# Kernel tuning notes

Measured on AMD Instinct MI355X. Metric: run time of the kernel, lower is better.

## Reference

```python
import jax, jax.numpy as jnp
import numpy as np

B, H, W = 16, 128, 128
CIN, HID, OUT = 1, 64, 1
WS, NH = 8, 4  # window size, num heads
HD = HID // NH  # head dim = 16


def setup_inputs() -> dict:
    key = jax.random.key(0)
    ks = jax.random.split(key, 32)
    s = 0.05
    d = {"x": jax.random.normal(ks[0], (B, H, W, CIN), jnp.float32)}
    ins = [CIN, HID]
    for l in range(2):
        cin = ins[l]
        kb = 1 + 7 * l
        d[f"conv_w{l}"] = jax.random.normal(ks[kb], (4 * HID, cin + HID, 3, 3), jnp.float32) * s
        d[f"conv_b{l}"] = jnp.zeros((4 * HID,), jnp.float32)
        d[f"px_w{l}"] = jax.random.normal(ks[kb + 1], (HID, cin, 3, 3), jnp.float32) * s
        d[f"py_w{l}"] = jax.random.normal(ks[kb + 2], (HID, cin, 3, 3), jnp.float32) * s
        d[f"qkv_w{l}"] = jax.random.normal(ks[kb + 3], (3 * HID, HID), jnp.float32) * s
        d[f"proj_w{l}"] = jax.random.normal(ks[kb + 4], (HID, HID), jnp.float32) * s
        d[f"proj_b{l}"] = jnp.zeros((HID,), jnp.float32)
    d["out_w"] = jax.random.normal(ks[20], (OUT, HID, 1, 1), jnp.float32) * s
    d["out_b"] = jnp.zeros((OUT,), jnp.float32)
    return d


def _conv(x, w, pad, b=None):
    y = jax.lax.conv_general_dilated(
        x, w, (1, 1), [(pad, pad), (pad, pad)],
        dimension_numbers=("NCHW", "OIHW", "NCHW"))
    if b is not None:
        y = y + b[None, :, None, None]
    return y


def _win_attn(x, qkv_w, proj_w, proj_b):
    # x: [B, H, W, C], H and W are multiples of WS (pad branch is a no-op)
    Bx, Hx, Wx, C = x.shape
    nw_h, nw_w = Hx // WS, Wx // WS
    xw = x.reshape(Bx, nw_h, WS, nw_w, WS, C).transpose(0, 1, 3, 2, 4, 5)
    xw = xw.reshape(-1, WS * WS, C)  # [N, T, C], N = B*nw_h*nw_w, T = 64
    qkv = (xw @ qkv_w.T).reshape(-1, WS * WS, 3, NH, HD).transpose(2, 0, 3, 1, 4)
    q, k, v = qkv[0], qkv[1], qkv[2]  # [N, NH, T, HD]
    attn = jax.nn.softmax(jnp.einsum("nhqd,nhkd->nhqk", q, k) * (HD ** -0.5), axis=-1)
    o = jnp.einsum("nhqk,nhkd->nhqd", attn, v).transpose(0, 2, 1, 3).reshape(-1, WS * WS, C)
    o = o @ proj_w.T + proj_b
    o = o.reshape(Bx, nw_h, nw_w, WS, WS, C).transpose(0, 1, 3, 2, 4, 5)
    return o.reshape(Bx, Hx, Wx, C)


def _cell(x, h, c, cw, cb, pxw, pyw, qw, pw, pb):
    # x: [B, Cin, H, W]; h, c: [B, HID, H, W]
    cc = _conv(jnp.concatenate([x, h], axis=1), cw, 1, cb)
    ci, cf, co, cg = jnp.split(cc, 4, axis=1)
    px = _conv(x, pxw, 1)
    py = _conv(x, pyw, 1)
    i = jax.nn.sigmoid(ci + px)
    f = jax.nn.sigmoid(cf + px)
    o = jax.nn.sigmoid(co + py)
    g = jnp.tanh(cg + py)
    c2 = f * c + i * g
    h2 = o * jnp.tanh(c2)
    h2 = _win_attn(h2.transpose(0, 2, 3, 1), qw, pw, pb).transpose(0, 3, 1, 2)
    return h2, c2


def reference(x, conv_w0, conv_b0, px_w0, py_w0, qkv_w0, proj_w0, proj_b0,
              conv_w1, conv_b1, px_w1, py_w1, qkv_w1, proj_w1, proj_b1,
              out_w, out_b):
    # 4D input path: [B,H,W,C] -> NCHW frame, seq_len = 1
    xin = x.transpose(0, 3, 1, 2)
    z = jnp.zeros((B, HID, H, W), x.dtype)
    h0, _ = _cell(xin, z, z, conv_w0, conv_b0, px_w0, py_w0, qkv_w0, proj_w0, proj_b0)
    h1, _ = _cell(h0, z, z, conv_w1, conv_b1, px_w1, py_w1, qkv_w1, proj_w1, proj_b1)
    out = _conv(h1, out_w, 0, out_b)  # 1x1 output conv on last layer's (T=1) output
    return out.transpose(0, 2, 3, 1)  # [B, H, W, OUT]
```

## Files before the change

### kernel.cpp

```cpp
#include <hip/hip_runtime.h>


#define DEVFN __device__ __forceinline__

typedef __attribute__((ext_vector_type(8))) short short8;
typedef __attribute__((ext_vector_type(4))) float f32x4;

DEVFN float sigmoidf_(float z) { return 1.0f / (1.0f + __expf(-z)); }

DEVFN float tanhf_(float x) {
    float e = __expf(2.0f * x);
    return 1.0f - 2.0f / (e + 1.0f);
}

DEVFN unsigned short f2bf(float f) {
    unsigned int u = __builtin_bit_cast(unsigned int, f);
    u += 0x7fffu + ((u >> 16) & 1u);
    return (unsigned short)(u >> 16);
}

DEVFN unsigned pkbf(float a, float b) {
    return (unsigned)f2bf(a) | ((unsigned)f2bf(b) << 16);
}

__global__ __launch_bounds__(256) void repack_kernel(
    const float* __restrict__ cw0, const float* __restrict__ pxw0, const float* __restrict__ pyw0,
    const float* __restrict__ cw1, const float* __restrict__ pxw1, const float* __restrict__ pyw1,
    const float* __restrict__ qkvw0, const float* __restrict__ projw0,
    const float* __restrict__ qkvw1, const float* __restrict__ projw1,
    unsigned short* __restrict__ pwc, float* __restrict__ pw0,
    unsigned short* __restrict__ qb0, unsigned short* __restrict__ pjb0,
    unsigned short* __restrict__ qb1, unsigned short* __restrict__ pjb1)
{
    int idx = blockIdx.x * 256 + threadIdx.x;
    if (idx < 184320) {
        int j = idx & 7;
        int lane = (idx >> 3) & 63;
        int wv = (idx >> 9) & 3;
        int t = idx >> 11;
        int kk = t % 18, g = t / 18;
        int c = wv * 16 + (lane & 15);
        int kcol = kk * 32 + (lane >> 4) * 8 + j;
        int pos = kcol >> 6, cin = kcol & 63;
        float v;
        if (g == 0)      v = cw1[((c      ) * 128 + cin) * 9 + pos];
        else if (g == 1) v = cw1[((128 + c) * 128 + cin) * 9 + pos];
        else if (g == 2) v = cw1[((192 + c) * 128 + cin) * 9 + pos];
        else if (g == 3) v = pxw1[(c * 64 + cin) * 9 + pos];
        else             v = pyw1[(c * 64 + cin) * 9 + pos];
        pwc[idx] = f2bf(v);
    } else if (idx < 187200) {
        int i2 = idx - 184320;
        int g = i2 / (9 * 64);
        int rem = i2 - g * (9 * 64);
        int pos = rem >> 6, c = rem & 63;
        float v;
        if (g == 0)      v = cw0[(c      ) * 585 + pos];
        else if (g == 1) v = cw0[(128 + c) * 585 + pos];
        else if (g == 2) v = cw0[(192 + c) * 585 + pos];
        else if (g == 3) v = pxw0[c * 9 + pos];
        else             v = pyw0[c * 9 + pos];
        pw0[i2] = v;
    } else if (idx < 187200 + 12288) {
        int i = idx - 187200;           qb0[i] = f2bf(qkvw0[i]);
    } else if (idx < 187200 + 24576) {
        int i = idx - 187200 - 12288;   qb1[i] = f2bf(qkvw1[i]);
    } else if (idx < 187200 + 24576 + 4096) {
        int i = idx - 187200 - 24576;   pjb0[i] = f2bf(projw0[i]);
    } else if (idx < 187200 + 24576 + 8192) {
        int i = idx - 187200 - 28672;   pjb1[i] = f2bf(projw1[i]);
    }
}

__global__ __launch_bounds__(256) void gates1_kernel(
    const float* __restrict__ x, const float* __restrict__ pw,
    const float* __restrict__ cb, unsigned short* __restrict__ dst)
{
    const int idx = blockIdx.x * 256 + threadIdx.x;
    const int pix = idx >> 4, ch0 = (idx & 15) * 4;
    const int b = pix >> 14, y = (pix >> 7) & 127, xq = pix & 127;

    float a[9];
#pragma unroll
    for (int dy = 0; dy < 3; ++dy)
#pragma unroll
        for (int dx = 0; dx < 3; ++dx) {
            int gy = y + dy - 1, gx = xq + dx - 1;
            a[dy * 3 + dx] = ((unsigned)gy < 128u && (unsigned)gx < 128u)
                ? x[(b * 128 + gy) * 128 + gx] : 0.f;
        }

    float acc[5][4];
#pragma unroll
    for (int g = 0; g < 5; ++g)
#pragma unroll
        for (int u = 0; u < 4; ++u) acc[g][u] = 0.f;

#pragma unroll
    for (int pos = 0; pos < 9; ++pos) {
        const float av = a[pos];
#pragma unroll
        for (int g = 0; g < 5; ++g) {
            const float4 w4 = *(const float4*)(pw + (g * 9 + pos) * 64 + ch0);
            acc[g][0] = fmaf(av, w4.x, acc[g][0]);
            acc[g][1] = fmaf(av, w4.y, acc[g][1]);
            acc[g][2] = fmaf(av, w4.z, acc[g][2]);
            acc[g][3] = fmaf(av, w4.w, acc[g][3]);
        }
    }

    float hv[4];
#pragma unroll
    for (int u = 0; u < 4; ++u) {
        float ci = acc[0][u] + cb[ch0 + u];
        float co = acc[1][u] + cb[128 + ch0 + u];
        float cg = acc[2][u] + cb[192 + ch0 + u];
        float iv = sigmoidf_(ci + acc[3][u]);
        float ov = sigmoidf_(co + acc[4][u]);
        float gv = tanhf_(cg + acc[4][u]);
        hv[u] = ov * tanhf_(iv * gv);
    }
    uint2 o;
    o.x = pkbf(hv[0], hv[1]);
    o.y = pkbf(hv[2], hv[3]);
    *(uint2*)(dst + (size_t)pix * 64 + ch0) = o;
}

__global__ __launch_bounds__(256, 2) void gates64_kernel(
    const unsigned short* __restrict__ src, const unsigned short* __restrict__ wtc,
    const float* __restrict__ cb, unsigned short* __restrict__ dst)
{
    __shared__ unsigned short lds[3 * 66 * 64];
    char* const sbase = (char*)lds;

    const int tid = threadIdx.x;
    const int bid = blockIdx.x;
    const int xt = bid & 1, y = (bid >> 1) & 127, b = bid >> 8;
    const int x0 = xt * 64;

    for (int i4 = tid; i4 < 3 * 66 * 8; i4 += 256) {
        int r = i4 / (66 * 8);
        int rem = i4 - r * (66 * 8);
        int xx = rem >> 3, c8 = rem & 7;
        int gy = y + r - 1, gx = x0 + xx - 1;
        uint4 wv = make_uint4(0, 0, 0, 0);
        if ((unsigned)gy < 128u && (unsigned)gx < 128u)
            wv = *(const uint4*)(src + (((size_t)(b * 128 + gy) * 128 + gx) * 64 + c8 * 8));
        int addr = ((r * 66 + xx) * 128 + c8 * 16) ^ ((xx & 7) << 4);
        *(uint4*)(sbase + addr) = wv;
    }
    __syncthreads();

    const int lane = tid & 63;
    const int wv_ = tid >> 6;
    const int r0 = lane & 15;
    const int hi = lane >> 4;
    const int wch = wv_ * 16 + r0;

    const unsigned short* wbase = wtc + (size_t)(wv_ * 64 + lane) * 8;

    f32x4 acc[4][5];
#pragma unroll
    for (int mt = 0; mt < 4; ++mt)
#pragma unroll
        for (int g = 0; g < 5; ++g) acc[mt][g] = (f32x4){0.f, 0.f, 0.f, 0.f};

#pragma unroll
    for (int kk = 0; kk < 18; ++kk) {
        const int pos = kk >> 1, dy = pos / 3, dx = pos % 3, chalf = kk & 1;
        const int swz = (((r0 + dx) & 7) << 4);
        short8 bfr[5];
#pragma unroll
        for (int g = 0; g < 5; ++g)
            bfr[g] = *(const short8*)(wbase + (g * 18 + kk) * 2048);
        short8 afr[4];
#pragma unroll
        for (int mt = 0; mt < 4; ++mt) {
            const int row = dy * 66 + mt * 16 + r0 + dx;
            const int addr = (row * 128 + chalf * 64 + hi * 16) ^ swz;
            afr[mt] = *(const short8*)(sbase + addr);
        }
#pragma unroll
        for (int mt = 0; mt < 4; ++mt)
#pragma unroll
            for (int g = 0; g < 5; ++g)
                acc[mt][g] = __builtin_amdgcn_mfma_f32_16x16x32_bf16(
                    afr[mt], bfr[g], acc[mt][g], 0, 0, 0);
    }

    const float bci = cb[wch], bco = cb[128 + wch], bcg = cb[192 + wch];
    const int rowbase = (b * 128 + y) * 128 + x0;
#pragma unroll
    for (int mt = 0; mt < 4; ++mt) {
#pragma unroll
        for (int rg = 0; rg < 4; ++rg) {
            const int px_i = mt * 16 + hi * 4 + rg;
            float ci = acc[mt][0][rg] + bci;
            float co = acc[mt][1][rg] + bco;
            float cg = acc[mt][2][rg] + bcg;
            float pxv = acc[mt][3][rg];
            float pyv = acc[mt][4][rg];
            float iv = sigmoidf_(ci + pxv);
            float ov = sigmoidf_(co + pyv);
            float gv = tanhf_(cg + pyv);
            dst[(size_t)(rowbase + px_i) * 64 + wch] = f2bf(ov * tanhf_(iv * gv));
        }
    }
}

template <int FUSE>
__global__ __launch_bounds__(256, 4) void attn_kernel(
    const unsigned short* __restrict__ src,
    const unsigned short* __restrict__ qkvwb,
    const unsigned short* __restrict__ projwb,
    const float* __restrict__ projb,
    unsigned short* __restrict__ dst,
    const float* __restrict__ outw,
    const float* __restrict__ outb,
    float* __restrict__ out)
{
    __shared__ char sm[32768];
    char* const Xs = sm;
    char* const Xo = sm + 8192;
    char* const Qs = sm + 16384;
    char* const Ks = sm + 19456;
    char* const VT = sm + 22528;
    char* const Ps = sm + 24576;

    const int tid = threadIdx.x;
    const int lane = tid & 63;
    const int w = __builtin_amdgcn_readfirstlane(tid >> 6);
    const int lo = lane & 15, hi = lane >> 4;
    const int wid = blockIdx.x;
    const int b = wid >> 8, rem = wid & 255, wy = rem >> 4, wx = rem & 15;
    const int pixbase = (b * 128 + wy * 8) * 128 + wx * 8;

    {
        const int t = tid >> 2, c0 = (tid & 3) * 16;
        const int pix = pixbase + (t >> 3) * 128 + (t & 7);
        const uint4* sp = (const uint4*)(src + (size_t)pix * 64 + c0);
        uint4 w0 = sp[0], w1 = sp[1];
        const int a = t * 128 + c0 * 2, sz = (t & 7) << 4;
        *(uint4*)(Xs + (a ^ sz)) = w0;
        *(uint4*)(Xs + ((a + 16) ^ sz)) = w1;
    }
    __syncthreads();

    const int trow = w * 16 + lo;
    const int tswz = (lo & 7) << 4;

    for (int h = 0; h < 4; ++h) {
        f32x4 cq = {0.f, 0.f, 0.f, 0.f}, ck = cq, cv = cq;
#pragma unroll
        for (int ks = 0; ks < 2; ++ks) {
            const int koff = hi * 8 + ks * 32;
            short8 xb = *(const short8*)(Xs + ((trow * 128 + koff * 2) ^ tswz));
            short8 aq = *(const short8*)(qkvwb + (h * 16 + lo) * 64 + koff);
            short8 ak = *(const short8*)(qkvwb + (64 + h * 16 + lo) * 64 + koff);
            short8 bv = *(const short8*)(qkvwb + (128 + h * 16 + lo) * 64 + koff);
            cq = __builtin_amdgcn_mfma_f32_16x16x32_bf16(aq, xb, cq, 0, 0, 0);
            ck = __builtin_amdgcn_mfma_f32_16x16x32_bf16(ak, xb, ck, 0, 0, 0);
            cv = __builtin_amdgcn_mfma_f32_16x16x32_bf16(xb, bv, cv, 0, 0, 0);
        }
        {
            uint2 qw, kw, vw;
            qw.x = pkbf(cq[0] * 0.125f, cq[1] * 0.125f);
            qw.y = pkbf(cq[2] * 0.125f, cq[3] * 0.125f);
            kw.x = pkbf(ck[0], ck[1]); kw.y = pkbf(ck[2], ck[3]);
            *(uint2*)(Qs + trow * 48 + hi * 8) = qw;
            *(uint2*)(Ks + trow * 48 + hi * 8) = kw;
            vw.x = pkbf(cv[0], cv[1]); vw.y = pkbf(cv[2], cv[3]);
            *(uint2*)(VT + ((lo * 128 + (w * 16 + hi * 4) * 2) ^ ((lo & 7) << 4))) = vw;
        }
        __syncthreads();

        short8 bq = *(const short8*)(Qs + trow * 48 + (hi & 1) * 16);
        f32x4 st[4];
#pragma unroll
        for (int mt = 0; mt < 4; ++mt) {
            short8 ak2 = *(const short8*)(Ks + (mt * 16 + lo) * 48 + (hi & 1) * 16);
            f32x4 z = {0.f, 0.f, 0.f, 0.f};
            st[mt] = __builtin_amdgcn_mfma_f32_16x16x32_bf16(ak2, bq, z, 0, 0, 0);
        }
        float mx = -1e30f;
#pragma unroll
        for (int mt = 0; mt < 4; ++mt)
#pragma unroll
            for (int r = 0; r < 4; ++r) mx = fmaxf(mx, st[mt][r]);
        mx = fmaxf(mx, __shfl_xor(mx, 16));
        mx = fmaxf(mx, __shfl_xor(mx, 32));
        float pv[16];
        float sum = 0.f;
#pragma unroll
        for (int mt = 0; mt < 4; ++mt)
#pragma unroll
            for (int r = 0; r < 4; ++r) {
                float e = __expf(st[mt][r] - mx);
                pv[mt * 4 + r] = e;
                sum += e;
            }
        sum += __shfl_xor(sum, 16);
        sum += __shfl_xor(sum, 32);
        const float rs = 1.0f / sum;
#pragma unroll
        for (int mt = 0; mt < 4; ++mt) {
            uint2 pw_;
            pw_.x = pkbf(pv[mt * 4 + 0] * rs, pv[mt * 4 + 1] * rs);
            pw_.y = pkbf(pv[mt * 4 + 2] * rs, pv[mt * 4 + 3] * rs);
            *(uint2*)(Ps + ((trow * 128 + (mt * 16 + hi * 4) * 2) ^ tswz)) = pw_;
        }

        f32x4 ot = {0.f, 0.f, 0.f, 0.f};
#pragma unroll
        for (int ks = 0; ks < 2; ++ks) {
            const int ko = (hi * 8 + ks * 32) * 2;
            short8 av = *(const short8*)(VT + ((lo * 128 + ko) ^ ((lo & 7) << 4)));
            short8 bp = *(const short8*)(Ps + ((trow * 128 + ko) ^ tswz));
            ot = __builtin_amdgcn_mfma_f32_16x16x32_bf16(av, bp, ot, 0, 0, 0);
        }
        {
            uint2 ow_;
            ow_.x = pkbf(ot[0], ot[1]); ow_.y = pkbf(ot[2], ot[3]);
            *(uint2*)(Xo + ((trow * 128 + (h * 16 + hi * 4) * 2) ^ tswz)) = ow_;
        }
        __syncthreads();
    }

    f32x4 cy[4];
#pragma unroll
    for (int mt = 0; mt < 4; ++mt) cy[mt] = (f32x4){0.f, 0.f, 0.f, 0.f};
#pragma unroll
    for (int ks = 0; ks < 2; ++ks) {
        const int koff = hi * 8 + ks * 32;
        short8 bw = *(const short8*)(projwb + (w * 16 + lo) * 64 + koff);
#pragma unroll
        for (int mt = 0; mt < 4; ++mt) {
            short8 ax = *(const short8*)(Xo + (((mt * 16 + lo) * 128 + koff * 2) ^ ((lo & 7) << 4)));
            cy[mt] = __builtin_amdgcn_mfma_f32_16x16x32_bf16(ax, bw, cy[mt], 0, 0, 0);
        }
    }
    const float pb = projb[w * 16 + lo];

    if constexpr (FUSE == 0) {
#pragma unroll
        for (int mt = 0; mt < 4; ++mt) {
#pragma unroll
            for (int r = 0; r < 4; ++r) {
                const int tok = mt * 16 + hi * 4 + r;
                const int pix = pixbase + (tok >> 3) * 128 + (tok & 7);
                dst[(size_t)pix * 64 + w * 16 + lo] = f2bf(cy[mt][r] + pb);
            }
        }
    } else {
        const float owv = outw[w * 16 + lo];
        float* red = (float*)VT;
#pragma unroll
        for (int mt = 0; mt < 4; ++mt) {
#pragma unroll
            for (int r = 0; r < 4; ++r) {
                float s = (cy[mt][r] + pb) * owv;
                s += __shfl_xor(s, 1);
                s += __shfl_xor(s, 2);
                s += __shfl_xor(s, 4);
                s += __shfl_xor(s, 8);
                if (lo == 0) red[(mt * 16 + hi * 4 + r) * 4 + w] = s;
            }
        }
        __syncthreads();
        if (tid < 64) {
            const int tok = tid;
            float4 rv = *(const float4*)(red + tok * 4);
            const int pix = pixbase + (tok >> 3) * 128 + (tok & 7);
            out[pix] = (rv.x + rv.y) + (rv.z + rv.w) + outb[0];
        }
    }
}

extern "C" void kernel_launch(void* const* d_in, const int* in_sizes, int n_in,
                              void* d_out, int out_size, void* d_ws, size_t ws_size,
                              hipStream_t stream)
{
    const float* x      = (const float*)d_in[0];
    const float* cw0    = (const float*)d_in[1];
    const float* cb0    = (const float*)d_in[2];
    const float* pxw0   = (const float*)d_in[3];
    const float* pyw0   = (const float*)d_in[4];
    const float* qkvw0  = (const float*)d_in[5];
    const float* projw0 = (const float*)d_in[6];
    const float* projb0 = (const float*)d_in[7];
    const float* cw1    = (const float*)d_in[8];
    const float* cb1    = (const float*)d_in[9];
    const float* pxw1   = (const float*)d_in[10];
    const float* pyw1   = (const float*)d_in[11];
    const float* qkvw1  = (const float*)d_in[12];
    const float* projw1 = (const float*)d_in[13];
    const float* projb1 = (const float*)d_in[14];
    const float* outw   = (const float*)d_in[15];
    const float* outb   = (const float*)d_in[16];

    const size_t BUF = (size_t)16 * 128 * 128 * 64 * sizeof(float);
    char* ws = (char*)d_ws;
    unsigned short* bufA = (unsigned short*)ws;
    unsigned short* bufB = (unsigned short*)(ws + BUF);
    char* wsx = ws + 2 * BUF;
    unsigned short* pwc  = (unsigned short*)(wsx);
    float* pw0           = (float*)(wsx + 369664);
    unsigned short* qb0  = (unsigned short*)(wsx + 381440);
    unsigned short* pjb0 = (unsigned short*)(wsx + 406016);
    unsigned short* qb1  = (unsigned short*)(wsx + 414208);
    unsigned short* pjb1 = (unsigned short*)(wsx + 438784);

    repack_kernel<<<860, 256, 0, stream>>>(
        cw0, pxw0, pyw0, cw1, pxw1, pyw1,
        qkvw0, projw0, qkvw1, projw1,
        pwc, pw0, qb0, pjb0, qb1, pjb1);

    gates1_kernel<<<16384, 256, 0, stream>>>(x, pw0, cb0, bufA);
    attn_kernel<0><<<4096, 256, 0, stream>>>(bufA, qb0, pjb0, projb0, bufB,
                                             nullptr, nullptr, nullptr);
    gates64_kernel<<<4096, 256, 0, stream>>>(bufB, pwc, cb1, bufA);
    attn_kernel<1><<<4096, 256, 0, stream>>>(bufA, qb1, pjb1, projb1, nullptr,
                                             outw, outb, (float*)d_out);
}
```

Measured before the change: 341.7 us.

## Batch all-head QKV projection before attention and widen gates64 blocks to full rows

```diff
diff --git a/kernel.cpp b/kernel.cpp
--- a/kernel.cpp
+++ b/kernel.cpp
@@ -36,10 +36,10 @@
     if (idx < 184320) {
         int j = idx & 7;
         int lane = (idx >> 3) & 63;
-        int wv = (idx >> 9) & 3;
+        int ng = (idx >> 9) & 3;
         int t = idx >> 11;
         int kk = t % 18, g = t / 18;
-        int c = wv * 16 + (lane & 15);
+        int c = ng * 16 + (lane & 15);
         int kcol = kk * 32 + (lane >> 4) * 8 + j;
         int pos = kcol >> 6, cin = kcol & 63;
         float v;
@@ -126,38 +126,39 @@
     *(uint2*)(dst + (size_t)pix * 64 + ch0) = o;
 }
 
-__global__ __launch_bounds__(256, 2) void gates64_kernel(
+__global__ __launch_bounds__(512, 2) void gates64_kernel(
     const unsigned short* __restrict__ src, const unsigned short* __restrict__ wtc,
     const float* __restrict__ cb, unsigned short* __restrict__ dst)
 {
-    __shared__ unsigned short lds[3 * 66 * 64];
+    __shared__ unsigned short lds[3 * 130 * 64];
     char* const sbase = (char*)lds;
 
     const int tid = threadIdx.x;
     const int bid = blockIdx.x;
-    const int xt = bid & 1, y = (bid >> 1) & 127, b = bid >> 8;
-    const int x0 = xt * 64;
-
-    for (int i4 = tid; i4 < 3 * 66 * 8; i4 += 256) {
-        int r = i4 / (66 * 8);
-        int rem = i4 - r * (66 * 8);
+    const int y = bid & 127, b = bid >> 7;
+
+    for (int i4 = tid; i4 < 3 * 130 * 8; i4 += 512) {
+        int r = i4 / (130 * 8);
+        int rem = i4 - r * (130 * 8);
         int xx = rem >> 3, c8 = rem & 7;
-        int gy = y + r - 1, gx = x0 + xx - 1;
+        int gy = y + r - 1, gx = xx - 1;
         uint4 wv = make_uint4(0, 0, 0, 0);
         if ((unsigned)gy < 128u && (unsigned)gx < 128u)
             wv = *(const uint4*)(src + (((size_t)(b * 128 + gy) * 128 + gx) * 64 + c8 * 8));
-        int addr = ((r * 66 + xx) * 128 + c8 * 16) ^ ((xx & 7) << 4);
+        int addr = ((r * 130 + xx) * 128 + c8 * 16) ^ ((xx & 7) << 4);
         *(uint4*)(sbase + addr) = wv;
     }
     __syncthreads();
 
     const int lane = tid & 63;
     const int wv_ = tid >> 6;
+    const int mg = wv_ >> 2;
+    const int ng = wv_ & 3;
     const int r0 = lane & 15;
     const int hi = lane >> 4;
-    const int wch = wv_ * 16 + r0;
-
-    const unsigned short* wbase = wtc + (size_t)(wv_ * 64 + lane) * 8;
+    const int wch = ng * 16 + r0;
+
+    const unsigned short* wbase = wtc + (size_t)(ng * 64 + lane) * 8;
 
     f32x4 acc[4][5];
 #pragma unroll
@@ -176,7 +177,7 @@
         short8 afr[4];
 #pragma unroll
         for (int mt = 0; mt < 4; ++mt) {
-            const int row = dy * 66 + mt * 16 + r0 + dx;
+            const int row = dy * 130 + mg * 64 + mt * 16 + r0 + dx;
             const int addr = (row * 128 + chalf * 64 + hi * 16) ^ swz;
             afr[mt] = *(const short8*)(sbase + addr);
         }
@@ -189,12 +190,12 @@
     }
 
     const float bci = cb[wch], bco = cb[128 + wch], bcg = cb[192 + wch];
-    const int rowbase = (b * 128 + y) * 128 + x0;
+    const int rowbase = (b * 128 + y) * 128;
 #pragma unroll
     for (int mt = 0; mt < 4; ++mt) {
 #pragma unroll
         for (int rg = 0; rg < 4; ++rg) {
-            const int px_i = mt * 16 + hi * 4 + rg;
+            const int px_i = mg * 64 + mt * 16 + hi * 4 + rg;
             float ci = acc[mt][0][rg] + bci;
             float co = acc[mt][1][rg] + bco;
             float cg = acc[mt][2][rg] + bcg;
@@ -209,7 +210,7 @@
 }
 
 template <int FUSE>
-__global__ __launch_bounds__(256, 4) void attn_kernel(
+__global__ __launch_bounds__(256, 3) void attn_kernel(
     const unsigned short* __restrict__ src,
     const unsigned short* __restrict__ qkvwb,
     const unsigned short* __restrict__ projwb,
@@ -219,13 +220,13 @@
     const float* __restrict__ outb,
     float* __restrict__ out)
 {
-    __shared__ char sm[32768];
+    __shared__ char sm[49152];
     char* const Xs = sm;
     char* const Xo = sm + 8192;
-    char* const Qs = sm + 16384;
-    char* const Ks = sm + 19456;
-    char* const VT = sm + 22528;
-    char* const Ps = sm + 24576;
+    char* const Qa = sm + 16384;
+    char* const Ka = sm + 24576;
+    char* const VT = sm + 32768;
+    char* const Ps = sm + 40960;
 
     const int tid = threadIdx.x;
     const int lane = tid & 63;
@@ -249,6 +250,7 @@
     const int trow = w * 16 + lo;
     const int tswz = (lo & 7) << 4;
 
+#pragma unroll
     for (int h = 0; h < 4; ++h) {
         f32x4 cq = {0.f, 0.f, 0.f, 0.f}, ck = cq, cv = cq;
 #pragma unroll
@@ -262,23 +264,25 @@
             ck = __builtin_amdgcn_mfma_f32_16x16x32_bf16(ak, xb, ck, 0, 0, 0);
             cv = __builtin_amdgcn_mfma_f32_16x16x32_bf16(xb, bv, cv, 0, 0, 0);
         }
-        {
-            uint2 qw, kw, vw;
-            qw.x = pkbf(cq[0] * 0.125f, cq[1] * 0.125f);
-            qw.y = pkbf(cq[2] * 0.125f, cq[3] * 0.125f);
-            kw.x = pkbf(ck[0], ck[1]); kw.y = pkbf(ck[2], ck[3]);
-            *(uint2*)(Qs + trow * 48 + hi * 8) = qw;
-            *(uint2*)(Ks + trow * 48 + hi * 8) = kw;
-            vw.x = pkbf(cv[0], cv[1]); vw.y = pkbf(cv[2], cv[3]);
-            *(uint2*)(VT + ((lo * 128 + (w * 16 + hi * 4) * 2) ^ ((lo & 7) << 4))) = vw;
-        }
-        __syncthreads();
-
-        short8 bq = *(const short8*)(Qs + trow * 48 + (hi & 1) * 16);
+        uint2 qw, kw, vw;
+        qw.x = pkbf(cq[0] * 0.125f, cq[1] * 0.125f);
+        qw.y = pkbf(cq[2] * 0.125f, cq[3] * 0.125f);
+        kw.x = pkbf(ck[0], ck[1]); kw.y = pkbf(ck[2], ck[3]);
+        vw.x = pkbf(cv[0], cv[1]); vw.y = pkbf(cv[2], cv[3]);
+        *(uint2*)(Qa + ((trow * 128 + (h * 16 + hi * 4) * 2) ^ tswz)) = qw;
+        *(uint2*)(Ka + ((trow * 128 + (h * 16 + hi * 4) * 2) ^ tswz)) = kw;
+        *(uint2*)(VT + (((h * 16 + lo) * 128 + (w * 16 + hi * 4) * 2) ^ ((lo & 7) << 4))) = vw;
+    }
+    __syncthreads();
+
+#pragma unroll 1
+    for (int h = 0; h < 4; ++h) {
+        const int hb = h * 32;
+        short8 bq = *(const short8*)(Qa + ((trow * 128 + hb + (hi & 1) * 16) ^ tswz));
         f32x4 st[4];
 #pragma unroll
         for (int mt = 0; mt < 4; ++mt) {
-            short8 ak2 = *(const short8*)(Ks + (mt * 16 + lo) * 48 + (hi & 1) * 16);
+            short8 ak2 = *(const short8*)(Ka + (((mt * 16 + lo) * 128 + hb + (hi & 1) * 16) ^ ((lo & 7) << 4)));
             f32x4 z = {0.f, 0.f, 0.f, 0.f};
             st[mt] = __builtin_amdgcn_mfma_f32_16x16x32_bf16(ak2, bq, z, 0, 0, 0);
         }
@@ -309,22 +313,19 @@
             pw_.y = pkbf(pv[mt * 4 + 2] * rs, pv[mt * 4 + 3] * rs);
             *(uint2*)(Ps + ((trow * 128 + (mt * 16 + hi * 4) * 2) ^ tswz)) = pw_;
         }
-
         f32x4 ot = {0.f, 0.f, 0.f, 0.f};
 #pragma unroll
         for (int ks = 0; ks < 2; ++ks) {
             const int ko = (hi * 8 + ks * 32) * 2;
-            short8 av = *(const short8*)(VT + ((lo * 128 + ko) ^ ((lo & 7) << 4)));
+            short8 av = *(const short8*)(VT + (((h * 16 + lo) * 128 + ko) ^ ((lo & 7) << 4)));
             short8 bp = *(const short8*)(Ps + ((trow * 128 + ko) ^ tswz));
             ot = __builtin_amdgcn_mfma_f32_16x16x32_bf16(av, bp, ot, 0, 0, 0);
         }
-        {
-            uint2 ow_;
-            ow_.x = pkbf(ot[0], ot[1]); ow_.y = pkbf(ot[2], ot[3]);
-            *(uint2*)(Xo + ((trow * 128 + (h * 16 + hi * 4) * 2) ^ tswz)) = ow_;
-        }
-        __syncthreads();
-    }
+        uint2 ow_;
+        ow_.x = pkbf(ot[0], ot[1]); ow_.y = pkbf(ot[2], ot[3]);
+        *(uint2*)(Xo + ((trow * 128 + (h * 16 + hi * 4) * 2) ^ tswz)) = ow_;
+    }
+    __syncthreads();
 
     f32x4 cy[4];
 #pragma unroll
@@ -418,7 +419,7 @@
     gates1_kernel<<<16384, 256, 0, stream>>>(x, pw0, cb0, bufA);
     attn_kernel<0><<<4096, 256, 0, stream>>>(bufA, qb0, pjb0, projb0, bufB,
                                              nullptr, nullptr, nullptr);
-    gates64_kernel<<<4096, 256, 0, stream>>>(bufB, pwc, cb1, bufA);
+    gates64_kernel<<<2048, 512, 0, stream>>>(bufB, pwc, cb1, bufA);
     attn_kernel<1><<<4096, 256, 0, stream>>>(bufA, qb1, pjb1, projb1, nullptr,
                                              outw, outb, (float*)d_out);
 }
```

Result: no change. 346.2 us (+1.3%).
